# Optimization experiments

Hardware: AMD Instinct MI355X
Metric: run time of the kernel (lower is better)

## Reference

```python
import jax, jax.numpy as jnp
import numpy as np
import math

QDIM = 512
KDIM = 512
MID = 512
MAIN_N = 2048
OTHER_N = 2048
BATCH = 32
NEG_BIG = -float(1 << 32)


def setup_inputs() -> dict:
    key = jax.random.key(0)
    ks = jax.random.split(key, 8)
    main_feat = jax.random.normal(ks[0], (MAIN_N, QDIM), dtype=jnp.float32)
    other_feat = jax.random.normal(ks[1], (OTHER_N, KDIM), dtype=jnp.float32)
    fix_feat = jax.random.uniform(ks[2], (BATCH, OTHER_N), dtype=jnp.float32)
    mask = jax.random.randint(ks[3], (MAIN_N, OTHER_N), 0, 2).astype(bool)
    # Linear params (PyTorch layout: W [out, in], b [out])
    sq = 1.0 / math.sqrt(QDIM)
    sk = 1.0 / math.sqrt(KDIM)
    Wq = jax.random.uniform(ks[4], (MID, QDIM), jnp.float32, -sq, sq)
    bq = jax.random.uniform(ks[5], (MID,), jnp.float32, -sq, sq)
    Wk = jax.random.uniform(ks[6], (MID, KDIM), jnp.float32, -sk, sk)
    bk = jax.random.uniform(ks[7], (MID,), jnp.float32, -sk, sk)
    return {"main_feat": main_feat, "other_feat": other_feat, "fix_feat": fix_feat,
            "mask": mask, "Wq": Wq, "bq": bq, "Wk": Wk, "bk": bk}


def reference(main_feat, other_feat, fix_feat, mask, Wq, bq, Wk, bk):
    # Q: [main, mid], K: [other, mid]
    Q = main_feat @ Wq.T + bq
    K = other_feat @ Wk.T + bk
    attn = (Q @ K.T) / math.sqrt(MID)            # [main, other]
    attn = jnp.where(mask, NEG_BIG, attn)
    attn = jax.nn.softmax(attn, axis=-1)
    # diag_embed(fix_feat) @ other_feat == per-token broadcast scale
    scaled = fix_feat[:, :, None] * other_feat[None, :, :]   # [batch, other, Kdim]
    return jnp.einsum('mo,bok->bmk', attn, scaled)           # [batch, main, Kdim]
```

## Files before the change

### kernel.cpp

```cpp
#include <hip/hip_runtime.h>
#include <hip/hip_bf16.h>

typedef unsigned short u16;
typedef __attribute__((ext_vector_type(8))) short short8;
typedef __attribute__((ext_vector_type(4))) float f32x4;

#define BATCH_ 32

static __device__ __forceinline__ float b2f(u16 u) {
  union { unsigned int i; float f; } v; v.i = ((unsigned int)u) << 16; return v.f;
}
static __device__ __forceinline__ u16 f2b(float x) {
  unsigned int i = __float_as_uint(x);
  unsigned int r = (i + 0x7fffu + ((i >> 16) & 1u)) >> 16;
  return (u16)r;
}

#define GCAST(p) ((const __attribute__((address_space(1))) void*)(p))
#define LCAST(p) ((__attribute__((address_space(3))) void*)(p))

__global__ __launch_bounds__(256) void cvt_bf16_dual(
    const float* __restrict__ s1, u16* __restrict__ d1, int n1,
    const float* __restrict__ s2, u16* __restrict__ d2, int n2) {
  int i = (blockIdx.x * 256 + threadIdx.x) * 4;
  const float* s; u16* d; int idx;
  if (i < n1) { s = s1; d = d1; idx = i; }
  else { idx = i - n1; if (idx >= n2) return; s = s2; d = d2; }
  float4 v = *(const float4*)(s + idx);
  ushort4 o;
  o.x = f2b(v.x); o.y = f2b(v.y); o.z = f2b(v.z); o.w = f2b(v.w);
  *(ushort4*)(d + idx) = o;
}

__global__ __launch_bounds__(256) void transpose_scale(
    const float* __restrict__ other, const float* __restrict__ fix,
    u16* __restrict__ scaled) {
  __shared__ float tile[32][33];
  __shared__ float fixs[32][33];
  int k0 = blockIdx.x * 32, o0 = blockIdx.y * 32;
  int tx = threadIdx.x & 31, ty = threadIdx.x >> 5;
  #pragma unroll
  for (int i = 0; i < 32; i += 8)
    tile[ty + i][tx] = other[(long long)(o0 + ty + i) * 512 + k0 + tx];
  #pragma unroll
  for (int i = 0; i < 32; i += 8)
    fixs[ty + i][tx] = fix[(long long)(ty + i) * 2048 + o0 + tx];
  __syncthreads();
  int kk = threadIdx.x >> 4;
  int oo = (threadIdx.x & 15) * 2;
  #pragma unroll 4
  for (int b = 0; b < 32; ++b) {
    #pragma unroll
    for (int p = 0; p < 2; ++p) {
      int k = kk + p * 16;
      ushort2 w;
      w.x = f2b(tile[oo][k] * fixs[b][oo]);
      w.y = f2b(tile[oo + 1][k] * fixs[b][oo + 1]);
      *(ushort2*)(scaled + ((long long)(b * 512 + k0 + k) * 2048 + o0 + oo)) = w;
    }
  }
}

__global__ __launch_bounds__(256) void softmax_mask(const u16* __restrict__ S,
                                                    const int* __restrict__ mask,
                                                    u16* __restrict__ P, int N) {
  const float scale = 0.044194173824159216f;
  int row = blockIdx.x;
  int t = threadIdx.x;
  long long base = (long long)row * N;
  float vals[8]; int msk[8];
  float mx = -3.0e38f;
  #pragma unroll
  for (int i = 0; i < 8; ++i) {
    int c = t + i * 256;
    float s = b2f(S[base + c]) * scale;
    int m = mask[base + c];
    vals[i] = s; msk[i] = m;
    if (!m) mx = fmaxf(mx, s);
  }
  #pragma unroll
  for (int off = 32; off; off >>= 1) mx = fmaxf(mx, __shfl_xor(mx, off));
  __shared__ float sred[4];
  if ((t & 63) == 0) sred[t >> 6] = mx;
  __syncthreads();
  mx = fmaxf(fmaxf(sred[0], sred[1]), fmaxf(sred[2], sred[3]));
  __syncthreads();
  float e[8]; float sum = 0.f;
  #pragma unroll
  for (int i = 0; i < 8; ++i) {
    e[i] = msk[i] ? 0.f : __expf(vals[i] - mx);
    sum += e[i];
  }
  #pragma unroll
  for (int off = 32; off; off >>= 1) sum += __shfl_xor(sum, off);
  if ((t & 63) == 0) sred[t >> 6] = sum;
  __syncthreads();
  sum = sred[0] + sred[1] + sred[2] + sred[3];
  float inv = (sum > 0.f) ? (1.f / sum) : 0.f;
  #pragma unroll
  for (int i = 0; i < 8; ++i) {
    int c = t + i * 256;
    P[base + c] = f2b(e[i] * inv);
  }
}

#define GBM 128
#define GBN 128
#define GBK 32

template<int EPI>
__global__ __launch_bounds__(256) void gemm_lds(
    const u16* __restrict__ A, const u16* __restrict__ Bt,
    const float* __restrict__ bias,
    const u16* __restrict__ Bt2, const float* __restrict__ bias2,
    float* __restrict__ outF, u16* __restrict__ outB,
    int M, int N, int K) {
  __shared__ u16 sA[GBM * GBK];
  __shared__ u16 sB[GBN * GBK];
  int m0 = blockIdx.y * GBM, n0 = blockIdx.x * GBN;
  if (EPI == 0) {
    if (2 * blockIdx.y >= gridDim.y) { Bt = Bt2; bias = bias2; }
  }
  int t = threadIdx.x;
  int wid = t >> 6, lane = t & 63;
  int wm = (wid >> 1) * 64, wn = (wid & 1) * 64;
  int lr = lane & 15, lq = lane >> 4;
  int srow = lane >> 2, schunk = (lane & 3) * 8;

  f32x4 acc[4][4];
  #pragma unroll
  for (int i = 0; i < 4; ++i)
    #pragma unroll
    for (int j = 0; j < 4; ++j)
      acc[i][j] = (f32x4){0.f, 0.f, 0.f, 0.f};

  const u16* gA = A + (long long)(m0 + wid * 32 + srow) * K + schunk;
  const u16* gB = Bt + (long long)(n0 + wid * 32 + srow) * K + schunk;
  u16* lA = &sA[(wid * 32) * GBK];
  u16* lB = &sB[(wid * 32) * GBK];
  const long long rowskip = (long long)16 * K;

  for (int k0 = 0; k0 < K; k0 += GBK) {
    __builtin_amdgcn_global_load_lds(GCAST(gA + k0),           LCAST(lA),            16, 0, 0);
    __builtin_amdgcn_global_load_lds(GCAST(gA + k0 + rowskip), LCAST(lA + 16 * GBK), 16, 0, 0);
    __builtin_amdgcn_global_load_lds(GCAST(gB + k0),           LCAST(lB),            16, 0, 0);
    __builtin_amdgcn_global_load_lds(GCAST(gB + k0 + rowskip), LCAST(lB + 16 * GBK), 16, 0, 0);
    __syncthreads();
    short8 af[4], bf[4];
    #pragma unroll
    for (int i = 0; i < 4; ++i)
      af[i] = *(const short8*)&sA[(wm + i * 16 + lr) * GBK + lq * 8];
    #pragma unroll
    for (int j = 0; j < 4; ++j)
      bf[j] = *(const short8*)&sB[(wn + j * 16 + lr) * GBK + lq * 8];
    #pragma unroll
    for (int i = 0; i < 4; ++i)
      #pragma unroll
      for (int j = 0; j < 4; ++j)
        acc[i][j] = __builtin_amdgcn_mfma_f32_16x16x32_bf16(af[i], bf[j], acc[i][j], 0, 0, 0);
    __syncthreads();
  }

  #pragma unroll
  for (int i = 0; i < 4; ++i) {
    #pragma unroll
    for (int j = 0; j < 4; ++j) {
      int col = n0 + wn + j * 16 + lr;
      #pragma unroll
      for (int r = 0; r < 4; ++r) {
        int row = m0 + wm + i * 16 + lq * 4 + r;
        float v = acc[i][j][r];
        if (EPI == 0) {
          outB[(long long)row * N + col] = f2b(v + bias[col]);
        } else if (EPI == 1) {
          outF[(long long)row * N + col] = v;
        } else {
          outB[(long long)row * N + col] = f2b(v);
        }
      }
    }
  }
}

#define SGB __builtin_amdgcn_sched_group_barrier

__global__ __launch_bounds__(512, 2) void gemm_ring(
    const u16* __restrict__ A, const u16* __restrict__ Bt,
    float* __restrict__ outF, int M, int N, int K) {
  __shared__ u16 lds[4][2][8192];

  int nwg = gridDim.x * gridDim.y;
  int wg = blockIdx.y * gridDim.x + blockIdx.x;
  int cpx = nwg >> 3;
  int swz = (wg & 7) * cpx + (wg >> 3);
  int bx = swz & 7, by = swz >> 3;
  int m0 = bx * 256, n0 = by * 256;

  int t = threadIdx.x;
  int w = t >> 6, lane = t & 63;
  int wr = w >> 2, wc = w & 3;
  int lr = lane & 15, lq = lane >> 4;
  int csw = (((lr >> 1) & 3) ^ lq) * 8;

  int srow = t >> 2;
  int sgc = (((srow >> 1) & 3) ^ (t & 3)) * 8;
  const u16* pA0 = A + (long long)(m0 + srow) * K + sgc;
  const u16* pA1 = pA0 + (long long)128 * K;
  const u16* pB0 = Bt + (long long)(n0 + srow) * K + sgc;
  const u16* pB1 = pB0 + (long long)128 * K;
  const int lbase = (w * 16) * 32;

  f32x4 acc[8][4];
  #pragma unroll
  for (int i = 0; i < 8; ++i)
    #pragma unroll
    for (int j = 0; j < 4; ++j)
      acc[i][j] = (f32x4){0.f, 0.f, 0.f, 0.f};

  const int NT = K >> 5;

  #define STAGE_TILE(KT, SB)                                                          \
    do {                                                                              \
      long long cofs = (long long)(KT) * 32;                                          \
      __builtin_amdgcn_global_load_lds(GCAST(pA0 + cofs), LCAST(&lds[SB][0][lbase]),            16, 0, 0); \
      __builtin_amdgcn_global_load_lds(GCAST(pA1 + cofs), LCAST(&lds[SB][0][lbase + 128 * 32]), 16, 0, 0); \
      __builtin_amdgcn_global_load_lds(GCAST(pB0 + cofs), LCAST(&lds[SB][1][lbase]),            16, 0, 0); \
      __builtin_amdgcn_global_load_lds(GCAST(pB1 + cofs), LCAST(&lds[SB][1][lbase + 128 * 32]), 16, 0, 0); \
    } while (0)

  #define RD_FRAGS(AF, BF, BUF) {                                                     \
    _Pragma("unroll")                                                                 \
    for (int i = 0; i < 8; ++i)                                                       \
      AF[i] = *(const short8*)&lds[BUF][0][(wr * 128 + i * 16 + lr) * 32 + csw];      \
    _Pragma("unroll")                                                                 \
    for (int j = 0; j < 4; ++j)                                                       \
      BF[j] = *(const short8*)&lds[BUF][1][(wc * 64 + j * 16 + lr) * 32 + csw]; }

  #define MFMA_NP(AF, BF) {                                                           \
    _Pragma("unroll")                                                                 \
    for (int i = 0; i < 8; ++i)                                                       \
      _Pragma("unroll")                                                               \
      for (int j = 0; j < 4; ++j)                                                     \
        acc[i][j] = __builtin_amdgcn_mfma_f32_16x16x32_bf16(AF[i], BF[j], acc[i][j], 0, 0, 0); }

  #define MFMA_BLK(AF, BF) {                                                          \
    __builtin_amdgcn_s_setprio(1);                                                    \
    MFMA_NP(AF, BF);                                                                  \
    __builtin_amdgcn_s_setprio(0); }

  #define SGB_TAIL() {                                                                \
    SGB(0x008, 2, 0);                                                                 \
    SGB(0x100, 2, 0); SGB(0x008, 4, 0);                                               \
    SGB(0x100, 2, 0); SGB(0x008, 4, 0);                                               \
    SGB(0x100, 2, 0); SGB(0x008, 4, 0);                                               \
    SGB(0x020, 4, 0);                                                                 \
    SGB(0x100, 2, 0); SGB(0x008, 4, 0);                                               \
    SGB(0x100, 2, 0); SGB(0x008, 4, 0);                                               \
    SGB(0x100, 2, 0); SGB(0x008, 4, 0);                                               \
    SGB(0x008, 6, 0); }

  short8 afA[8], bfA[4], afB[8], bfB[4];

  STAGE_TILE(0, 0);
  STAGE_TILE(1, 1);
  STAGE_TILE(2, 2);
  asm volatile("s_waitcnt vmcnt(4)" ::: "memory");
  __builtin_amdgcn_s_barrier();
  __builtin_amdgcn_sched_barrier(0);
  RD_FRAGS(afA, bfA, 0);

  for (int kt = 0; kt + 4 < NT; kt += 2) {
    RD_FRAGS(afB, bfB, ((kt + 1) & 3));
    STAGE_TILE(kt + 3, ((kt + 3) & 3));
    MFMA_NP(afA, bfA);
    SGB_TAIL();
    asm volatile("s_waitcnt vmcnt(4)" ::: "memory");
    __builtin_amdgcn_s_barrier();
    __builtin_amdgcn_sched_barrier(0);
    RD_FRAGS(afA, bfA, ((kt + 2) & 3));
    STAGE_TILE(kt + 4, ((kt + 4) & 3));
    MFMA_NP(afB, bfB);
    SGB_TAIL();
    asm volatile("s_waitcnt vmcnt(4)" ::: "memory");
    __builtin_amdgcn_s_barrier();
    __builtin_amdgcn_sched_barrier(0);
  }

  RD_FRAGS(afB, bfB, ((NT - 3) & 3));
  STAGE_TILE(NT - 1, ((NT - 1) & 3));
  __builtin_amdgcn_sched_barrier(0);
  MFMA_BLK(afA, bfA);
  __builtin_amdgcn_sched_barrier(0);
  asm volatile("s_waitcnt vmcnt(4)" ::: "memory");
  __builtin_amdgcn_s_barrier();
  __builtin_amdgcn_sched_barrier(0);
  RD_FRAGS(afA, bfA, ((NT - 2) & 3));
  __builtin_amdgcn_sched_barrier(0);
  MFMA_BLK(afB, bfB);
  __builtin_amdgcn_sched_barrier(0);
  asm volatile("s_waitcnt vmcnt(0)" ::: "memory");
  __builtin_amdgcn_s_barrier();
  __builtin_amdgcn_sched_barrier(0);
  RD_FRAGS(afB, bfB, ((NT - 1) & 3));
  __builtin_amdgcn_sched_barrier(0);
  MFMA_BLK(afA, bfA);
  MFMA_BLK(afB, bfB);

  #undef STAGE_TILE
  #undef RD_FRAGS
  #undef MFMA_NP
  #undef MFMA_BLK
  #undef SGB_TAIL

  #pragma unroll
  for (int i = 0; i < 8; ++i) {
    #pragma unroll
    for (int j = 0; j < 4; ++j) {
      int col = n0 + wc * 64 + j * 16 + lr;
      int b = col >> 9, kc = col & 511;
      float* ob = outF + (long long)b * ((long long)M * 512) + kc;
      #pragma unroll
      for (int r = 0; r < 4; ++r) {
        int row = m0 + wr * 128 + i * 16 + lq * 4 + r;
        ob[(long long)row * 512] = acc[i][j][r];
      }
    }
  }
}

__global__ __launch_bounds__(256) void transpose_cvt(const float* __restrict__ src,
                                                     u16* __restrict__ dst, int R, int C) {
  __shared__ float tile[32][33];
  int c0 = blockIdx.x * 32, r0 = blockIdx.y * 32;
  int tx = threadIdx.x & 31, ty = threadIdx.x >> 5;
  #pragma unroll
  for (int i = 0; i < 32; i += 8)
    tile[ty + i][tx] = src[(long long)(r0 + ty + i) * C + c0 + tx];
  __syncthreads();
  #pragma unroll
  for (int i = 0; i < 32; i += 8)
    dst[(long long)(c0 + ty + i) * R + r0 + tx] = f2b(tile[tx][ty + i]);
}

#define BMT 128
#define BNT 128
#define BKT 32
#define LDSP 40

template<int MODE>
__global__ __launch_bounds__(256) void gemm_bt(
    const u16* __restrict__ A, const u16* __restrict__ Bt,
    const float* __restrict__ bias, const float* __restrict__ fixmat,
    float* __restrict__ outF, u16* __restrict__ outB,
    int M, int N, int K, long long out_batch_stride, int bt_batch_stride) {
  __shared__ u16 sA[BMT][LDSP];
  __shared__ u16 sB[BNT][LDSP];
  int b = blockIdx.z;
  const u16* Bt_b = Bt + (long long)b * bt_batch_stride;
  const float* fixrow = (MODE == 2) ? (fixmat + (long long)b * K) : nullptr;
  float* out_b = (MODE == 1 || MODE == 2) ? (outF + (long long)b * out_batch_stride) : nullptr;

  int m0 = blockIdx.y * BMT, n0 = blockIdx.x * BNT;
  int t = threadIdx.x;
  int wid = t >> 6, lane = t & 63;
  int wm = (wid >> 1) * 64, wn = (wid & 1) * 64;
  int lr = lane & 15, lq = lane >> 4;

  f32x4 acc[4][4];
  #pragma unroll
  for (int i = 0; i < 4; ++i)
    #pragma unroll
    for (int j = 0; j < 4; ++j)
      acc[i][j] = (f32x4){0.f, 0.f, 0.f, 0.f};

  int srow = t >> 1, scg = (t & 1) * 16;

  for (int k0 = 0; k0 < K; k0 += BKT) {
    {
      const u16* src = A + (long long)(m0 + srow) * K + k0 + scg;
      short8 v0 = *(const short8*)(src);
      short8 v1 = *(const short8*)(src + 8);
      *(short8*)&sA[srow][scg] = v0;
      *(short8*)&sA[srow][scg + 8] = v1;
    }
    {
      const u16* src = Bt_b + (long long)(n0 + srow) * K + k0 + scg;
      short8 v0 = *(const short8*)(src);
      short8 v1 = *(const short8*)(src + 8);
      if (MODE == 2) {
        u16* p0 = (u16*)&v0; u16* p1 = (u16*)&v1;
        #pragma unroll
        for (int j = 0; j < 8; ++j) {
          p0[j] = f2b(b2f(p0[j]) * fixrow[k0 + scg + j]);
          p1[j] = f2b(b2f(p1[j]) * fixrow[k0 + scg + 8 + j]);
        }
      }
      *(short8*)&sB[srow][scg] = v0;
      *(short8*)&sB[srow][scg + 8] = v1;
    }
    __syncthreads();
    short8 af[4], bf[4];
    #pragma unroll
    for (int i = 0; i < 4; ++i)
      af[i] = *(const short8*)&sA[wm + i * 16 + lr][lq * 8];
    #pragma unroll
    for (int j = 0; j < 4; ++j)
      bf[j] = *(const short8*)&sB[wn + j * 16 + lr][lq * 8];
    #pragma unroll
    for (int i = 0; i < 4; ++i)
      #pragma unroll
      for (int j = 0; j < 4; ++j)
        acc[i][j] = __builtin_amdgcn_mfma_f32_16x16x32_bf16(af[i], bf[j], acc[i][j], 0, 0, 0);
    __syncthreads();
  }

  #pragma unroll
  for (int i = 0; i < 4; ++i) {
    #pragma unroll
    for (int j = 0; j < 4; ++j) {
      int col = n0 + wn + j * 16 + lr;
      #pragma unroll
      for (int r = 0; r < 4; ++r) {
        int row = m0 + wm + i * 16 + lq * 4 + r;
        float v = acc[i][j][r];
        if (MODE == 0) {
          v += bias[col];
          outB[(long long)row * N + col] = f2b(v);
        } else if (MODE == 3) {
          outB[(long long)row * N + col] = f2b(v);
        } else {
          out_b[(long long)row * N + col] = v;
        }
      }
    }
  }
}

extern "C" void kernel_launch(void* const* d_in, const int* in_sizes, int n_in,
                              void* d_out, int out_size, void* d_ws, size_t ws_size,
                              hipStream_t stream) {
  const float* main_feat  = (const float*)d_in[0];
  const float* other_feat = (const float*)d_in[1];
  const float* fix_feat   = (const float*)d_in[2];
  const int*   mask       = (const int*)d_in[3];
  const float* Wq         = (const float*)d_in[4];
  const float* bq         = (const float*)d_in[5];
  const float* Wk         = (const float*)d_in[6];
  const float* bk         = (const float*)d_in[7];
  float* out = (float*)d_out;

  char* ws = (char*)d_ws;
  const size_t OFF_MAINB  = 0;
  const size_t OFF_OTHERB = 2097152;
  const size_t OFF_WQB    = 4194304;
  const size_t OFF_WKB    = 4718592;
  const size_t OFF_QB     = 5242880;
  const size_t OFF_KB     = 7340032;
  const size_t OFF_OTB    = 9437184;
  const size_t OFF_P      = 11534336;
  const size_t OFF_S      = 19922944;
  const size_t OFF_SCALED = 36700160;
  const size_t NEED_SCALED = OFF_SCALED + (size_t)BATCH_ * 512 * 2048 * 2;

  u16* mainB  = (u16*)(ws + OFF_MAINB);
  u16* otherB = (u16*)(ws + OFF_OTHERB);
  u16* WqB    = (u16*)(ws + OFF_WQB);
  u16* WkB    = (u16*)(ws + OFF_WKB);
  u16* QB     = (u16*)(ws + OFF_QB);
  u16* KB     = (u16*)(ws + OFF_KB);
  u16* oTB    = (u16*)(ws + OFF_OTB);
  u16* P      = (u16*)(ws + OFF_P);
  u16* S      = (u16*)(ws + OFF_S);
  u16* scaled = (u16*)(ws + OFF_SCALED);
  bool use_scaled = (ws_size >= NEED_SCALED);

  cvt_bf16_dual<<<2048, 256, 0, stream>>>(main_feat, mainB, 2048 * 512,
                                          other_feat, otherB, 2048 * 512);
  cvt_bf16_dual<<<512, 256, 0, stream>>>(Wq, WqB, 512 * 512,
                                         Wk, WkB, 512 * 512);

  if (use_scaled) {
    transpose_scale<<<dim3(16, 64), 256, 0, stream>>>(other_feat, fix_feat, scaled);
    gemm_lds<0><<<dim3(4, 32), 256, 0, stream>>>(mainB, WqB, bq, WkB, bk,
        nullptr, QB, 4096, 512, 512);
    gemm_lds<3><<<dim3(16, 16), 256, 0, stream>>>(QB, KB, nullptr, nullptr, nullptr,
        nullptr, S, 2048, 2048, 512);
    softmax_mask<<<2048, 256, 0, stream>>>(S, mask, P, 2048);
    gemm_ring<<<dim3(8, 64), 512, 0, stream>>>(P, scaled, out, 2048, 16384, 2048);
  } else {
    transpose_cvt<<<dim3(16, 64), 256, 0, stream>>>(other_feat, oTB, 2048, 512);
    gemm_bt<0><<<dim3(4, 16, 1), 256, 0, stream>>>(mainB, WqB, bq, nullptr,
        nullptr, QB, 2048, 512, 512, 0, 0);
    gemm_bt<0><<<dim3(4, 16, 1), 256, 0, stream>>>(otherB, WkB, bk, nullptr,
        nullptr, KB, 2048, 512, 512, 0, 0);
    gemm_bt<3><<<dim3(16, 16, 1), 256, 0, stream>>>(QB, KB, nullptr, nullptr,
        nullptr, S, 2048, 2048, 512, 0, 0);
    softmax_mask<<<2048, 256, 0, stream>>>(S, mask, P, 2048);
    gemm_bt<2><<<dim3(4, 16, BATCH_), 256, 0, stream>>>(P, oTB, nullptr, fix_feat,
        out, nullptr, 2048, 512, 2048, 1048576LL, 0);
  }
}
```

Baseline: 177.0 us.

## Restructure ring GEMM into 64-wide K tiles with quadrant ping-pong phases

Replaces the 4-slot ring of 32-wide K tiles with a double-buffered layout of 64-wide K tiles. Each tile is split into A/B halves that are staged at a finer grain and interleaved with four quadrant MFMA phases separated by barriers, in the style of an 8-wave ping-pong schedule. The LDS swizzle changes to an 8-way XOR over 64-element rows. This cuts the number of loop iterations and is meant to overlap global-to-LDS loads with matrix math more evenly. In exchange it adds many more barriers per iteration and drops the hand-tuned sched_group_barrier interleave.

```diff
diff --git a/kernel.cpp b/kernel.cpp
--- a/kernel.cpp
+++ b/kernel.cpp
@@ -182,12 +182,10 @@
   }
 }
 
-#define SGB __builtin_amdgcn_sched_group_barrier
-
 __global__ __launch_bounds__(512, 2) void gemm_ring(
     const u16* __restrict__ A, const u16* __restrict__ Bt,
     float* __restrict__ outF, int M, int N, int K) {
-  __shared__ u16 lds[4][2][8192];
+  __shared__ u16 lds[65536];
 
   int nwg = gridDim.x * gridDim.y;
   int wg = blockIdx.y * gridDim.x + blockIdx.x;
@@ -200,15 +198,14 @@
   int w = t >> 6, lane = t & 63;
   int wr = w >> 2, wc = w & 3;
   int lr = lane & 15, lq = lane >> 4;
-  int csw = (((lr >> 1) & 3) ^ lq) * 8;
-
-  int srow = t >> 2;
-  int sgc = (((srow >> 1) & 3) ^ (t & 3)) * 8;
-  const u16* pA0 = A + (long long)(m0 + srow) * K + sgc;
-  const u16* pA1 = pA0 + (long long)128 * K;
-  const u16* pB0 = Bt + (long long)(n0 + srow) * K + sgc;
-  const u16* pB1 = pB0 + (long long)128 * K;
-  const int lbase = (w * 16) * 32;
+  const int s0 = (lq ^ (lr & 7)) * 8;
+  const int s1 = s0 ^ 32;
+
+  int rloc = t >> 3;
+  int cch = ((t & 7) ^ (rloc & 7)) * 8;
+  const u16* pAs = A + (long long)(m0 + rloc) * K + cch;
+  const u16* pBs = Bt + (long long)(n0 + rloc) * K + cch;
+  const int w512 = w * 512;
 
   f32x4 acc[8][4];
   #pragma unroll
@@ -217,100 +214,109 @@
     for (int j = 0; j < 4; ++j)
       acc[i][j] = (f32x4){0.f, 0.f, 0.f, 0.f};
 
-  const int NT = K >> 5;
-
-  #define STAGE_TILE(KT, SB)                                                          \
-    do {                                                                              \
-      long long cofs = (long long)(KT) * 32;                                          \
-      __builtin_amdgcn_global_load_lds(GCAST(pA0 + cofs), LCAST(&lds[SB][0][lbase]),            16, 0, 0); \
-      __builtin_amdgcn_global_load_lds(GCAST(pA1 + cofs), LCAST(&lds[SB][0][lbase + 128 * 32]), 16, 0, 0); \
-      __builtin_amdgcn_global_load_lds(GCAST(pB0 + cofs), LCAST(&lds[SB][1][lbase]),            16, 0, 0); \
-      __builtin_amdgcn_global_load_lds(GCAST(pB1 + cofs), LCAST(&lds[SB][1][lbase + 128 * 32]), 16, 0, 0); \
-    } while (0)
-
-  #define RD_FRAGS(AF, BF, BUF) {                                                     \
+  #define STG_H(OP, D, H, KT) do {                                                    \
+    const u16* sp_ = (OP) ? pBs : pAs;                                                \
+    long long ro_ = (long long)((H) * 128) * K + (long long)(KT) * 64;                \
+    int db_ = (D) * 32768 + (OP) * 16384 + (H) * 128 * 64 + w512;                     \
+    __builtin_amdgcn_global_load_lds(GCAST(sp_ + ro_),          LCAST(&lds[db_]),        16, 0, 0); \
+    __builtin_amdgcn_global_load_lds(GCAST(sp_ + ro_ + 64 * K), LCAST(&lds[db_ + 4096]), 16, 0, 0); \
+  } while (0)
+
+  #define RDA(DST, RI, D) {                                                           \
     _Pragma("unroll")                                                                 \
-    for (int i = 0; i < 8; ++i)                                                       \
-      AF[i] = *(const short8*)&lds[BUF][0][(wr * 128 + i * 16 + lr) * 32 + csw];      \
+    for (int ii = 0; ii < 4; ++ii) {                                                  \
+      int ro_ = (D) * 32768 + (wr * 128 + ((RI) * 4 + ii) * 16 + lr) * 64;            \
+      DST[ii * 2]     = *(const short8*)&lds[ro_ + s0];                               \
+      DST[ii * 2 + 1] = *(const short8*)&lds[ro_ + s1];                               \
+    } }
+
+  #define RDB(DST, CJ, D) {                                                           \
     _Pragma("unroll")                                                                 \
-    for (int j = 0; j < 4; ++j)                                                       \
-      BF[j] = *(const short8*)&lds[BUF][1][(wc * 64 + j * 16 + lr) * 32 + csw]; }
-
-  #define MFMA_NP(AF, BF) {                                                           \
+    for (int jj = 0; jj < 2; ++jj) {                                                  \
+      int ro_ = (D) * 32768 + 16384 + (wc * 64 + ((CJ) * 2 + jj) * 16 + lr) * 64;     \
+      DST[jj * 2]     = *(const short8*)&lds[ro_ + s0];                               \
+      DST[jj * 2 + 1] = *(const short8*)&lds[ro_ + s1];                               \
+    } }
+
+  #define MFQ(RI, CJ, AF, BF) {                                                       \
+    __builtin_amdgcn_s_setprio(1);                                                    \
     _Pragma("unroll")                                                                 \
-    for (int i = 0; i < 8; ++i)                                                       \
+    for (int ii = 0; ii < 4; ++ii)                                                    \
       _Pragma("unroll")                                                               \
-      for (int j = 0; j < 4; ++j)                                                     \
-        acc[i][j] = __builtin_amdgcn_mfma_f32_16x16x32_bf16(AF[i], BF[j], acc[i][j], 0, 0, 0); }
-
-  #define MFMA_BLK(AF, BF) {                                                          \
-    __builtin_amdgcn_s_setprio(1);                                                    \
-    MFMA_NP(AF, BF);                                                                  \
+      for (int jj = 0; jj < 2; ++jj)                                                  \
+        _Pragma("unroll")                                                             \
+        for (int kh = 0; kh < 2; ++kh)                                                \
+          acc[(RI) * 4 + ii][(CJ) * 2 + jj] = __builtin_amdgcn_mfma_f32_16x16x32_bf16(\
+              AF[ii * 2 + kh], BF[jj * 2 + kh], acc[(RI) * 4 + ii][(CJ) * 2 + jj], 0, 0, 0); \
     __builtin_amdgcn_s_setprio(0); }
 
-  #define SGB_TAIL() {                                                                \
-    SGB(0x008, 2, 0);                                                                 \
-    SGB(0x100, 2, 0); SGB(0x008, 4, 0);                                               \
-    SGB(0x100, 2, 0); SGB(0x008, 4, 0);                                               \
-    SGB(0x100, 2, 0); SGB(0x008, 4, 0);                                               \
-    SGB(0x020, 4, 0);                                                                 \
-    SGB(0x100, 2, 0); SGB(0x008, 4, 0);                                               \
-    SGB(0x100, 2, 0); SGB(0x008, 4, 0);                                               \
-    SGB(0x100, 2, 0); SGB(0x008, 4, 0);                                               \
-    SGB(0x008, 6, 0); }
-
-  short8 afA[8], bfA[4], afB[8], bfB[4];
-
-  STAGE_TILE(0, 0);
-  STAGE_TILE(1, 1);
-  STAGE_TILE(2, 2);
-  asm volatile("s_waitcnt vmcnt(4)" ::: "memory");
-  __builtin_amdgcn_s_barrier();
-  __builtin_amdgcn_sched_barrier(0);
-  RD_FRAGS(afA, bfA, 0);
-
-  for (int kt = 0; kt + 4 < NT; kt += 2) {
-    RD_FRAGS(afB, bfB, ((kt + 1) & 3));
-    STAGE_TILE(kt + 3, ((kt + 3) & 3));
-    MFMA_NP(afA, bfA);
-    SGB_TAIL();
-    asm volatile("s_waitcnt vmcnt(4)" ::: "memory");
-    __builtin_amdgcn_s_barrier();
-    __builtin_amdgcn_sched_barrier(0);
-    RD_FRAGS(afA, bfA, ((kt + 2) & 3));
-    STAGE_TILE(kt + 4, ((kt + 4) & 3));
-    MFMA_NP(afB, bfB);
-    SGB_TAIL();
-    asm volatile("s_waitcnt vmcnt(4)" ::: "memory");
-    __builtin_amdgcn_s_barrier();
-    __builtin_amdgcn_sched_barrier(0);
-  }
-
-  RD_FRAGS(afB, bfB, ((NT - 3) & 3));
-  STAGE_TILE(NT - 1, ((NT - 1) & 3));
-  __builtin_amdgcn_sched_barrier(0);
-  MFMA_BLK(afA, bfA);
-  __builtin_amdgcn_sched_barrier(0);
-  asm volatile("s_waitcnt vmcnt(4)" ::: "memory");
-  __builtin_amdgcn_s_barrier();
-  __builtin_amdgcn_sched_barrier(0);
-  RD_FRAGS(afA, bfA, ((NT - 2) & 3));
-  __builtin_amdgcn_sched_barrier(0);
-  MFMA_BLK(afB, bfB);
-  __builtin_amdgcn_sched_barrier(0);
+  #define SB0 __builtin_amdgcn_sched_barrier(0)
+  #define BAR __builtin_amdgcn_s_barrier()
+  #define PH_SYNC() do { SB0; BAR;                                                    \
+    asm volatile("s_waitcnt lgkmcnt(0)" ::: "memory"); SB0; } while (0)
+
+  short8 a0[8], a1[8], b0[4], b1[4];
+
+  STG_H(0, 0, 0, 0); STG_H(0, 0, 1, 0); STG_H(1, 0, 0, 0); STG_H(1, 0, 1, 0);
+  STG_H(0, 1, 0, 1); STG_H(0, 1, 1, 1); STG_H(1, 1, 0, 1); STG_H(1, 1, 1, 1);
   asm volatile("s_waitcnt vmcnt(0)" ::: "memory");
-  __builtin_amdgcn_s_barrier();
-  __builtin_amdgcn_sched_barrier(0);
-  RD_FRAGS(afB, bfB, ((NT - 1) & 3));
-  __builtin_amdgcn_sched_barrier(0);
-  MFMA_BLK(afA, bfA);
-  MFMA_BLK(afB, bfB);
-
-  #undef STAGE_TILE
-  #undef RD_FRAGS
-  #undef MFMA_NP
-  #undef MFMA_BLK
-  #undef SGB_TAIL
+  BAR; SB0;
+
+  const int NIT = K >> 7;
+  for (int it = 0; it < NIT; ++it) {
+    const int a = it * 2;
+    const bool first = (it == 0), last = (it == NIT - 1);
+    RDA(a0, 0, 0); RDB(b0, 0, 0);
+    if (!first) STG_H(0, 1, 0, a + 1);
+    PH_SYNC();
+    MFQ(0, 0, a0, b0);
+    SB0; BAR;
+    RDB(b1, 1, 0);
+    if (!first) STG_H(0, 1, 1, a + 1);
+    PH_SYNC();
+    MFQ(0, 1, a0, b1);
+    SB0; BAR;
+    RDA(a1, 1, 0);
+    if (!last) STG_H(1, 0, 0, a + 2);
+    PH_SYNC();
+    MFQ(1, 0, a1, b0);
+    SB0; BAR;
+    if (!last) STG_H(1, 0, 1, a + 2);
+    SB0; BAR; SB0;
+    MFQ(1, 1, a1, b1);
+    SB0;
+    if (!last) { asm volatile("s_waitcnt vmcnt(4)" ::: "memory"); }
+    else       { asm volatile("s_waitcnt vmcnt(0)" ::: "memory"); }
+    BAR; SB0;
+    RDA(a0, 0, 1); RDB(b0, 0, 1);
+    if (!last) STG_H(0, 0, 0, a + 2);
+    PH_SYNC();
+    MFQ(0, 0, a0, b0);
+    SB0; BAR;
+    RDB(b1, 1, 1);
+    if (!last) STG_H(0, 0, 1, a + 2);
+    PH_SYNC();
+    MFQ(0, 1, a0, b1);
+    SB0; BAR;
+    RDA(a1, 1, 1);
+    if (!last) STG_H(1, 1, 0, a + 3);
+    PH_SYNC();
+    MFQ(1, 0, a1, b0);
+    SB0; BAR;
+    if (!last) STG_H(1, 1, 1, a + 3);
+    SB0; BAR; SB0;
+    MFQ(1, 1, a1, b1);
+    SB0;
+    if (!last) { asm volatile("s_waitcnt vmcnt(4)" ::: "memory"); BAR; SB0; }
+  }
+
+  #undef STG_H
+  #undef RDA
+  #undef RDB
+  #undef MFQ
+  #undef SB0
+  #undef BAR
+  #undef PH_SYNC
 
   #pragma unroll
   for (int i = 0; i < 8; ++i) {
```

After: 177.3 us. No clear change (+0.1%).
